# Kernel tuning notes

Hardware: AMD Instinct MI355X
Metric: run time of the kernel (lower is better)

The kernel has to match this reference:

```python
import jax, jax.numpy as jnp
import numpy as np
import math

B, L, H, NH = 4, 1024, 512, 8
D = H // NH

def setup_inputs() -> dict:
    key = jax.random.key(0)
    ks = jax.random.split(key, 12)
    s = 1.0 / math.sqrt(H)
    return {
        "key": jax.random.normal(ks[0], (B, L, H), jnp.float32),
        "query": jax.random.normal(ks[1], (B, L, H), jnp.float32),
        "value": jax.random.normal(ks[2], (B, L, H), jnp.float32),
        "rel_pos_embedding": jax.random.normal(ks[3], (B, NH, L, L), jnp.float32),
        "wk_w": jax.random.normal(ks[4], (H, H), jnp.float32) * s,
        "wk_b": jnp.zeros((H,), jnp.float32),
        "wq_w": jax.random.normal(ks[5], (H, H), jnp.float32) * s,
        "wq_b": jnp.zeros((H,), jnp.float32),
        "wv_w": jax.random.normal(ks[6], (H, H), jnp.float32) * s,
        "wv_b": jnp.zeros((H,), jnp.float32),
        "ff_w": jax.random.normal(ks[7], (H, H), jnp.float32) * s,
        "ff_b": jnp.zeros((H,), jnp.float32),
        "seq_len": jax.random.randint(ks[8], (B,), 1, 768, jnp.int32),
        "lex_num": jax.random.randint(ks[9], (B,), 0, 256, jnp.int32),
    }

def reference(key, query, value, rel_pos_embedding, wk_w, wk_b, wq_w, wq_b, wv_w, wv_b, ff_w, ff_b, seq_len, lex_num):
    b, l, h = key.shape
    # projections (torch Linear: x @ W^T + b)
    k = (key @ wk_w.T + wk_b).reshape(b, l, NH, D)
    q = (query @ wq_w.T + wq_b).reshape(b, l, NH, D)
    v = (value @ wv_w.T + wv_b).reshape(b, l, NH, D)
    # QK^T: [b, nh, lq, lk]
    scores = jnp.einsum("bqhd,bkhd->bhqk", q, k) / math.sqrt(D)
    scores = scores + rel_pos_embedding
    # padding mask over key positions
    lengths = (seq_len + lex_num).astype(jnp.int32)  # [b]
    mask = jnp.arange(l, dtype=jnp.int32)[None, :] < lengths[:, None]  # [b, l]
    scores = jnp.where(mask[:, None, None, :], scores, jnp.float32(-1e15))
    attn = jax.nn.softmax(scores, axis=-1)
    out = jnp.einsum("bhqk,bkhd->bqhd", attn, v).reshape(b, l, h)
    out = out @ ff_w.T + ff_b
    return out
```

## Files before the change

### kernel.cpp

```cpp
#include <hip/hip_runtime.h>
#include <hip/hip_bf16.h>

typedef __attribute__((ext_vector_type(8))) short bf16x8;
typedef __attribute__((ext_vector_type(4))) float f32x4;

__device__ __forceinline__ unsigned short f2bf(float f) {
    return __builtin_bit_cast(unsigned short, __float2bfloat16(f));
}

typedef const __attribute__((address_space(1))) void gvoid;
typedef __attribute__((address_space(3))) void lvoid;
#define GLDS(g, s) __builtin_amdgcn_global_load_lds((gvoid*)(g), (lvoid*)(s), 16, 0, 0)

__device__ __forceinline__ void block_barrier() {
    asm volatile("" ::: "memory");
    __builtin_amdgcn_s_barrier();
    asm volatile("" ::: "memory");
}

__global__ __launch_bounds__(256) void proj_kernel(
    const float* __restrict__ query, const float* __restrict__ key_, const float* __restrict__ value,
    const float* __restrict__ wq_w, const float* __restrict__ wq_b,
    const float* __restrict__ wk_w, const float* __restrict__ wk_b,
    const float* __restrict__ wv_w, const float* __restrict__ wv_b,
    unsigned short* __restrict__ Qb, unsigned short* __restrict__ Kb, unsigned short* __restrict__ Vt)
{
    const int wid = (blockIdx.x & 7) * 96 + (blockIdx.x >> 3);
    const int z  = wid >> 8;
    const int rr = wid & 255;
    const int by = rr >> 3, bx = rr & 7;

    const float* X    = (z == 0) ? query : (z == 1) ? key_ : value;
    const float* W    = (z == 0) ? wq_w  : (z == 1) ? wk_w : wv_w;
    const float* bias = (z == 0) ? wq_b  : (z == 1) ? wk_b : wv_b;

    const int t = threadIdx.x;
    const int l = t & 63;
    const int w = t >> 6;
    const int wm = w >> 1, wn = w & 1;
    const int m0 = by * 128, n0 = bx * 64;

    __shared__ __align__(16) unsigned short As[128 * 32];
    __shared__ __align__(16) unsigned short Bs[64 * 32];

    f32x4 acc[4][2];
#pragma unroll
    for (int i = 0; i < 4; i++)
#pragma unroll
        for (int j = 0; j < 2; j++) acc[i][j] = (f32x4){0.f, 0.f, 0.f, 0.f};

    float4 ra[4], rb[2];
    auto LOAD = [&](int k0) {
#pragma unroll
        for (int i = 0; i < 4; i++) {
            int idx = t + 256 * i;
            int row = idx >> 3, c = idx & 7;
            ra[i] = *(const float4*)(X + (size_t)(m0 + row) * 512 + k0 + c * 4);
        }
#pragma unroll
        for (int i = 0; i < 2; i++) {
            int idx = t + 256 * i;
            int row = idx >> 3, c = idx & 7;
            rb[i] = *(const float4*)(W + (size_t)(n0 + row) * 512 + k0 + c * 4);
        }
    };
    LOAD(0);

    for (int k0 = 0; k0 < 512; k0 += 32) {
        if (k0) block_barrier();
#pragma unroll
        for (int i = 0; i < 4; i++) {
            int idx = t + 256 * i;
            int row = idx >> 3, c = idx & 7;
            __align__(8) unsigned short va[4] = {f2bf(ra[i].x), f2bf(ra[i].y), f2bf(ra[i].z), f2bf(ra[i].w)};
            *(uint2*)(As + row * 32 + (((c >> 1) ^ (row & 3)) * 8) + (c & 1) * 4) = *(uint2*)va;
        }
#pragma unroll
        for (int i = 0; i < 2; i++) {
            int idx = t + 256 * i;
            int row = idx >> 3, c = idx & 7;
            __align__(8) unsigned short vb[4] = {f2bf(rb[i].x), f2bf(rb[i].y), f2bf(rb[i].z), f2bf(rb[i].w)};
            *(uint2*)(Bs + row * 32 + (((c >> 1) ^ (row & 3)) * 8) + (c & 1) * 4) = *(uint2*)vb;
        }
        asm volatile("s_waitcnt lgkmcnt(0)" ::: "memory");
        block_barrier();
        if (k0 + 32 < 512) LOAD(k0 + 32);

        bf16x8 af[4], bfv[2];
#pragma unroll
        for (int mf = 0; mf < 4; mf++) {
            int row = wm * 64 + mf * 16 + (l & 15);
            af[mf] = *(const bf16x8*)(As + row * 32 + (((l >> 4) ^ (row & 3)) * 8));
        }
#pragma unroll
        for (int nf = 0; nf < 2; nf++) {
            int row = wn * 32 + nf * 16 + (l & 15);
            bfv[nf] = *(const bf16x8*)(Bs + row * 32 + (((l >> 4) ^ (row & 3)) * 8));
        }
#pragma unroll
        for (int mf = 0; mf < 4; mf++)
#pragma unroll
            for (int nf = 0; nf < 2; nf++)
                acc[mf][nf] = __builtin_amdgcn_mfma_f32_16x16x32_bf16(af[mf], bfv[nf], acc[mf][nf], 0, 0, 0);
    }

    if (z < 2) {
        unsigned short* dst = (z == 0) ? Qb : Kb;
#pragma unroll
        for (int nf = 0; nf < 2; nf++) {
            int n = n0 + wn * 32 + nf * 16 + (l & 15);
            float bv = bias[n];
            int h = n >> 6, d = n & 63;
#pragma unroll
            for (int mf = 0; mf < 4; mf++) {
                int mbase = m0 + wm * 64 + mf * 16 + 4 * (l >> 4);
                int bb = mbase >> 10;
#pragma unroll
                for (int r = 0; r < 4; r++) {
                    int lq = (mbase + r) & 1023;
                    dst[((size_t)(bb * 8 + h) * 1024 + lq) * 64 + d] = f2bf(acc[mf][nf][r] + bv);
                }
            }
        }
    } else {
#pragma unroll
        for (int nf = 0; nf < 2; nf++) {
            int n = n0 + wn * 32 + nf * 16 + (l & 15);
            float bv = bias[n];
            int h = n >> 6, d = n & 63;
#pragma unroll
            for (int mf = 0; mf < 4; mf++) {
                int mbase = m0 + wm * 64 + mf * 16 + 4 * (l >> 4);
                int bb = mbase >> 10;
                int lq0 = mbase & 1023;
                ushort4 pk;
                pk.x = f2bf(acc[mf][nf][0] + bv);
                pk.y = f2bf(acc[mf][nf][1] + bv);
                pk.z = f2bf(acc[mf][nf][2] + bv);
                pk.w = f2bf(acc[mf][nf][3] + bv);
                *(ushort4*)(Vt + ((size_t)(bb * 8 + h) * 64 + d) * 1024 + lq0) = pk;
            }
        }
    }
}

__global__ __launch_bounds__(256, 2) void attn_kernel(
    const unsigned short* __restrict__ Qb, const unsigned short* __restrict__ Kb,
    const unsigned short* __restrict__ Vt, const float* __restrict__ rel_pos,
    const int* __restrict__ seq_len, const int* __restrict__ lex_num,
    unsigned short* __restrict__ AO)
{
    const int t = threadIdx.x;
    const int l = t & 63;
    const int w = t >> 6;
    const int wid = (blockIdx.x & 7) * 64 + (blockIdx.x >> 3);
    const int x8 = wid >> 6;
    const int g  = (wid >> 4) & 3;
    const int qt = wid & 15;
    const int b  = g;
    const int h  = (x8 + 2 * g) & 7;
    const int q0 = qt * 64;
    const int bh = b * 8 + h;
    const int len = seq_len[b] + lex_num[b];
    const int nkt = (len + 127) >> 7;

    __shared__ __align__(16) unsigned short Qs[64 * 64];
    __shared__ __align__(16) unsigned short Ks[2][128 * 64];
    __shared__ __align__(16) unsigned short Vs[64 * 128];
    __shared__ __align__(16) unsigned short Ps[4 * 16 * 128];

    const unsigned short* Qg = Qb + ((size_t)bh * 1024 + q0) * 64;
    const unsigned short* Kg = Kb + (size_t)bh * 1024 * 64;
    const unsigned short* Vg = Vt + (size_t)bh * 64 * 1024;
    const float* Rg = rel_pos + ((size_t)bh * 1024 + q0) * 1024;

    const int rl8 = l >> 3, c8 = l & 7;
    const int kvc = (c8 ^ rl8) * 8;
    const int rl4 = l >> 4, c16 = l & 15;

    auto STAGE_K = [&](int kt2, int nb) {
        const int k0s = kt2 * 128;
#pragma unroll
        for (int j = 0; j < 4; j++) {
            int row = j * 32 + w * 8 + rl8;
            GLDS(Kg + (size_t)(k0s + row) * 64 + kvc, &Ks[nb][(j * 32 + w * 8) * 64]);
        }
    };
    auto STAGE_V = [&](int kt2) {
        const int k0s = kt2 * 128;
#pragma unroll
        for (int j = 0; j < 4; j++) {
            int drow = j * 16 + w * 4 + rl4;
            int sc = (c16 ^ (w * 4 + rl4)) * 8;
            GLDS(Vg + (size_t)drow * 1024 + k0s + sc, &Vs[(j * 16 + w * 4) * 128]);
        }
    };
    auto RELLOAD = [&](float (&R)[32], int kt2) {
        const float* rp = Rg + (size_t)(w * 16 + 4 * (l >> 4)) * 1024 + kt2 * 128 + (l & 15);
#pragma unroll
        for (int r = 0; r < 4; r++)
#pragma unroll
            for (int kn = 0; kn < 8; kn++)
                R[r * 8 + kn] = rp[(size_t)r * 1024 + kn * 16];
    };

    float rA[32], rB[32];
#pragma unroll
    for (int j = 0; j < 2; j++) {
        int row = w * 16 + j * 8 + rl8;
        GLDS(Qg + (size_t)row * 64 + kvc, &Qs[(w * 16 + j * 8) * 64]);
    }
    STAGE_K(0, 0);
    RELLOAD(rA, 0);
    STAGE_V(0);

    bf16x8 qf[2];
    f32x4 oacc[4];
#pragma unroll
    for (int dn = 0; dn < 4; dn++) oacc[dn] = (f32x4){0.f, 0.f, 0.f, 0.f};
    float l_run[4] = {0.f, 0.f, 0.f, 0.f};
    unsigned short* Pw = Ps + w * 16 * 128;

    auto tile_body = [&](int kt, float (&REL)[32], float (&RELN)[32]) {
        const int cur = kt & 1;
        const int k0 = kt * 128;
        if (kt + 1 < nkt) {
            STAGE_K(kt + 1, cur ^ 1);
            RELLOAD(RELN, kt + 1);
            asm volatile("s_waitcnt vmcnt(40)" ::: "memory");
        } else {
            asm volatile("s_waitcnt vmcnt(4)" ::: "memory");
        }
        block_barrier();

        if (kt == 0) {
#pragma unroll
            for (int s = 0; s < 2; s++) {
                int row = w * 16 + (l & 15);
                int ch = 4 * s + (l >> 4);
                qf[s] = *(const bf16x8*)(Qs + row * 64 + ((ch ^ (row & 7)) * 8));
            }
        }

        const unsigned short* Ksc = Ks[cur];

        f32x4 sa[8];
#pragma unroll
        for (int kn = 0; kn < 8; kn++) sa[kn] = (f32x4){0.f, 0.f, 0.f, 0.f};
        __builtin_amdgcn_s_setprio(1);
#pragma unroll
        for (int s = 0; s < 2; s++)
#pragma unroll
            for (int kn = 0; kn < 8; kn++) {
                int krow = kn * 16 + (l & 15);
                int ch = 4 * s + (l >> 4);
                bf16x8 kf = *(const bf16x8*)(Ksc + krow * 64 + ((ch ^ (krow & 7)) * 8));
                sa[kn] = __builtin_amdgcn_mfma_f32_16x16x32_bf16(qf[s], kf, sa[kn], 0, 0, 0);
            }
        __builtin_amdgcn_s_setprio(0);

#pragma unroll
        for (int r = 0; r < 4; r++) {
            int qrow = 4 * (l >> 4) + r;
            float pr[8], rs = 0.f;
#pragma unroll
            for (int kn = 0; kn < 8; kn++) {
                int kg = k0 + kn * 16 + (l & 15);
                float x = sa[kn][r] * 0.125f + REL[r * 8 + kn] - 16.0f;
                pr[kn] = (kg < len) ? __expf(x) : 0.0f;
                rs += pr[kn];
            }
#pragma unroll
            for (int o = 1; o < 16; o <<= 1) rs += __shfl_xor(rs, o, 64);
            l_run[r] += rs;
#pragma unroll
            for (int kn = 0; kn < 8; kn++) {
                int ck = (kn * 2 + ((l >> 3) & 1)) ^ (qrow & 15);
                Pw[qrow * 128 + ck * 8 + (l & 7)] = f2bf(pr[kn]);
            }
        }

        if (kt + 1 < nkt) {
            asm volatile("s_waitcnt vmcnt(36)" ::: "memory");
        } else {
            asm volatile("s_waitcnt vmcnt(0)" ::: "memory");
        }
        block_barrier();

        __builtin_amdgcn_s_setprio(1);
#pragma unroll
        for (int s = 0; s < 4; s++) {
            int arow = (l & 15);
            bf16x8 pf = *(const bf16x8*)(Pw + arow * 128 + (((s * 4 + (l >> 4)) ^ arow) * 8));
#pragma unroll
            for (int dn = 0; dn < 4; dn++) {
                int drow = dn * 16 + (l & 15);
                bf16x8 vf = *(const bf16x8*)(Vs + drow * 128 + (((s * 4 + (l >> 4)) ^ (drow & 15)) * 8));
                oacc[dn] = __builtin_amdgcn_mfma_f32_16x16x32_bf16(pf, vf, oacc[dn], 0, 0, 0);
            }
        }
        __builtin_amdgcn_s_setprio(0);
        block_barrier();
        if (kt + 1 < nkt) STAGE_V(kt + 1);
    };

    for (int kt = 0; kt < nkt; kt += 2) {
        tile_body(kt, rA, rB);
        if (kt + 1 < nkt) tile_body(kt + 1, rB, rA);
    }

    unsigned short* AOg = AO + ((size_t)(b * 1024 + q0 + w * 16)) * 512 + h * 64;
#pragma unroll
    for (int r = 0; r < 4; r++) {
        float inv = 1.0f / l_run[r];
        int qrow = 4 * (l >> 4) + r;
#pragma unroll
        for (int dn = 0; dn < 4; dn++)
            AOg[(size_t)qrow * 512 + dn * 16 + (l & 15)] = f2bf(oacc[dn][r] * inv);
    }
}

__global__ __launch_bounds__(256) void ff_kernel(
    const unsigned short* __restrict__ AO, const float* __restrict__ ff_w,
    const float* __restrict__ ff_b, float* __restrict__ out)
{
    const int t = threadIdx.x;
    const int l = t & 63;
    const int w = t >> 6;
    const int wm = w >> 1, wn = w & 1;
    const int wid = (blockIdx.x & 7) * 64 + (blockIdx.x >> 3);
    const int by = wid >> 3;
    const int bx = wid & 7;
    const int m0 = by * 64, n0 = bx * 64;

    __shared__ __align__(16) unsigned short As[64 * 32];
    __shared__ __align__(16) unsigned short Bs[64 * 32];

    f32x4 acc[2][2];
#pragma unroll
    for (int i = 0; i < 2; i++)
#pragma unroll
        for (int j = 0; j < 2; j++) acc[i][j] = (f32x4){0.f, 0.f, 0.f, 0.f};

    uint4 ua;
    float4 rbf[2];
    const int arow = t >> 2, ac = t & 3;
    auto LOAD = [&](int k0) {
        ua = *(const uint4*)(AO + (size_t)(m0 + arow) * 512 + k0 + ac * 8);
#pragma unroll
        for (int i = 0; i < 2; i++) {
            int idx = t + 256 * i;
            int row = idx >> 3, c = idx & 7;
            rbf[i] = *(const float4*)(ff_w + (size_t)(n0 + row) * 512 + k0 + c * 4);
        }
    };
    LOAD(0);

    for (int k0 = 0; k0 < 512; k0 += 32) {
        if (k0) block_barrier();
        *(uint4*)(As + arow * 32 + ((ac ^ (arow & 3)) * 8)) = ua;
#pragma unroll
        for (int i = 0; i < 2; i++) {
            int idx = t + 256 * i;
            int row = idx >> 3, c = idx & 7;
            __align__(8) unsigned short vb[4] = {f2bf(rbf[i].x), f2bf(rbf[i].y), f2bf(rbf[i].z), f2bf(rbf[i].w)};
            *(uint2*)(Bs + row * 32 + (((c >> 1) ^ (row & 3)) * 8) + (c & 1) * 4) = *(uint2*)vb;
        }
        asm volatile("s_waitcnt lgkmcnt(0)" ::: "memory");
        block_barrier();
        if (k0 + 32 < 512) LOAD(k0 + 32);

        bf16x8 af[2], bfv[2];
#pragma unroll
        for (int mf = 0; mf < 2; mf++) {
            int row = wm * 32 + mf * 16 + (l & 15);
            af[mf] = *(const bf16x8*)(As + row * 32 + (((l >> 4) ^ (row & 3)) * 8));
        }
#pragma unroll
        for (int nf = 0; nf < 2; nf++) {
            int row = wn * 32 + nf * 16 + (l & 15);
            bfv[nf] = *(const bf16x8*)(Bs + row * 32 + (((l >> 4) ^ (row & 3)) * 8));
        }
#pragma unroll
        for (int mf = 0; mf < 2; mf++)
#pragma unroll
            for (int nf = 0; nf < 2; nf++)
                acc[mf][nf] = __builtin_amdgcn_mfma_f32_16x16x32_bf16(af[mf], bfv[nf], acc[mf][nf], 0, 0, 0);
    }

#pragma unroll
    for (int nf = 0; nf < 2; nf++) {
        int n = n0 + wn * 32 + nf * 16 + (l & 15);
        float bv = ff_b[n];
#pragma unroll
        for (int mf = 0; mf < 2; mf++) {
            int mbase = m0 + wm * 32 + mf * 16 + 4 * (l >> 4);
#pragma unroll
            for (int r = 0; r < 4; r++)
                out[(size_t)(mbase + r) * 512 + n] = acc[mf][nf][r] + bv;
        }
    }
}

extern "C" void kernel_launch(void* const* d_in, const int* in_sizes, int n_in,
                              void* d_out, int out_size, void* d_ws, size_t ws_size,
                              hipStream_t stream) {
    const float* key   = (const float*)d_in[0];
    const float* query = (const float*)d_in[1];
    const float* value = (const float*)d_in[2];
    const float* rel   = (const float*)d_in[3];
    const float* wk_w  = (const float*)d_in[4];
    const float* wk_b  = (const float*)d_in[5];
    const float* wq_w  = (const float*)d_in[6];
    const float* wq_b  = (const float*)d_in[7];
    const float* wv_w  = (const float*)d_in[8];
    const float* wv_b  = (const float*)d_in[9];
    const float* ff_w  = (const float*)d_in[10];
    const float* ff_b  = (const float*)d_in[11];
    const int* seq_len = (const int*)d_in[12];
    const int* lex_num = (const int*)d_in[13];
    float* out = (float*)d_out;

    unsigned short* Qb = (unsigned short*)d_ws;
    unsigned short* Kb = Qb + 2097152;
    unsigned short* Vt = Kb + 2097152;
    unsigned short* AO = Vt + 2097152;

    proj_kernel<<<dim3(768), 256, 0, stream>>>(query, key, value,
                                               wq_w, wq_b, wk_w, wk_b, wv_w, wv_b,
                                               Qb, Kb, Vt);
    attn_kernel<<<dim3(512), 256, 0, stream>>>(Qb, Kb, Vt, rel, seq_len, lex_num, AO);
    ff_kernel<<<dim3(512), 256, 0, stream>>>(AO, ff_w, ff_b, out);
}
```

Before: 57.52 us.

## Stage fp32 projection tiles via async global-to-LDS loads with double buffering

The projection GEMM now loads fp32 tiles of X and W straight into LDS with global_load_lds into two ping-pong buffers, using an XOR swizzle. The bf16 conversion moves to after the LDS read, where each thread converts its own fragments. The goal is to overlap the next tile's global load with the current MFMA work and to drop the register round-trip and conversion stores. In exchange it uses twice the LDS (fp32, double-buffered), which can lower occupancy, repeats the conversions per wave, and adds a second barrier per iteration.

```diff
diff --git a/kernel.cpp b/kernel.cpp
--- a/kernel.cpp
+++ b/kernel.cpp
@@ -40,8 +40,8 @@
     const int wm = w >> 1, wn = w & 1;
     const int m0 = by * 128, n0 = bx * 64;
 
-    __shared__ __align__(16) unsigned short As[128 * 32];
-    __shared__ __align__(16) unsigned short Bs[64 * 32];
+    __shared__ __align__(16) float Asf[2][128 * 32];
+    __shared__ __align__(16) float Bsf[2][64 * 32];
 
     f32x4 acc[4][2];
 #pragma unroll
@@ -49,59 +49,66 @@
 #pragma unroll
         for (int j = 0; j < 2; j++) acc[i][j] = (f32x4){0.f, 0.f, 0.f, 0.f};
 
-    float4 ra[4], rb[2];
-    auto LOAD = [&](int k0) {
-#pragma unroll
-        for (int i = 0; i < 4; i++) {
-            int idx = t + 256 * i;
-            int row = idx >> 3, c = idx & 7;
-            ra[i] = *(const float4*)(X + (size_t)(m0 + row) * 512 + k0 + c * 4);
-        }
-#pragma unroll
-        for (int i = 0; i < 2; i++) {
-            int idx = t + 256 * i;
-            int row = idx >> 3, c = idx & 7;
-            rb[i] = *(const float4*)(W + (size_t)(n0 + row) * 512 + k0 + c * 4);
-        }
-    };
-    LOAD(0);
-
-    for (int k0 = 0; k0 < 512; k0 += 32) {
-        if (k0) block_barrier();
-#pragma unroll
-        for (int i = 0; i < 4; i++) {
-            int idx = t + 256 * i;
-            int row = idx >> 3, c = idx & 7;
-            __align__(8) unsigned short va[4] = {f2bf(ra[i].x), f2bf(ra[i].y), f2bf(ra[i].z), f2bf(ra[i].w)};
-            *(uint2*)(As + row * 32 + (((c >> 1) ^ (row & 3)) * 8) + (c & 1) * 4) = *(uint2*)va;
-        }
-#pragma unroll
-        for (int i = 0; i < 2; i++) {
-            int idx = t + 256 * i;
-            int row = idx >> 3, c = idx & 7;
-            __align__(8) unsigned short vb[4] = {f2bf(rb[i].x), f2bf(rb[i].y), f2bf(rb[i].z), f2bf(rb[i].w)};
-            *(uint2*)(Bs + row * 32 + (((c >> 1) ^ (row & 3)) * 8) + (c & 1) * 4) = *(uint2*)vb;
-        }
-        asm volatile("s_waitcnt lgkmcnt(0)" ::: "memory");
-        block_barrier();
-        if (k0 + 32 < 512) LOAD(k0 + 32);
+    const int rl8 = l >> 3, c8 = l & 7;
+    const int csrc = (c8 ^ rl8) * 4;
+
+    auto STAGE = [&](int kt, int nb) {
+        const int k0 = kt * 32;
+#pragma unroll
+        for (int j = 0; j < 4; j++) {
+            int row = j * 32 + w * 8 + rl8;
+            GLDS(X + (size_t)(m0 + row) * 512 + k0 + csrc, &Asf[nb][(j * 32 + w * 8) * 32]);
+        }
+#pragma unroll
+        for (int j = 0; j < 2; j++) {
+            int row = j * 32 + w * 8 + rl8;
+            GLDS(W + (size_t)(n0 + row) * 512 + k0 + csrc, &Bsf[nb][(j * 32 + w * 8) * 32]);
+        }
+    };
+
+    STAGE(0, 0);
+
+    for (int kt = 0; kt < 16; kt++) {
+        const int cur = kt & 1;
+        if (kt + 1 < 16) {
+            STAGE(kt + 1, cur ^ 1);
+            asm volatile("s_waitcnt vmcnt(6)" ::: "memory");
+        } else {
+            asm volatile("s_waitcnt vmcnt(0)" ::: "memory");
+        }
+        block_barrier();
+
+        const float* Ac = Asf[cur];
+        const float* Bc = Bsf[cur];
+        const int ch2 = 2 * (l >> 4);
+        const int s = l & 7;
 
         bf16x8 af[4], bfv[2];
 #pragma unroll
         for (int mf = 0; mf < 4; mf++) {
             int row = wm * 64 + mf * 16 + (l & 15);
-            af[mf] = *(const bf16x8*)(As + row * 32 + (((l >> 4) ^ (row & 3)) * 8));
+            float4 lo = *(const float4*)(Ac + row * 32 + ((ch2 ^ s) * 4));
+            float4 hi = *(const float4*)(Ac + row * 32 + (((ch2 + 1) ^ s) * 4));
+            __align__(16) unsigned short v[8] = {f2bf(lo.x), f2bf(lo.y), f2bf(lo.z), f2bf(lo.w),
+                                                 f2bf(hi.x), f2bf(hi.y), f2bf(hi.z), f2bf(hi.w)};
+            af[mf] = *(const bf16x8*)v;
         }
 #pragma unroll
         for (int nf = 0; nf < 2; nf++) {
             int row = wn * 32 + nf * 16 + (l & 15);
-            bfv[nf] = *(const bf16x8*)(Bs + row * 32 + (((l >> 4) ^ (row & 3)) * 8));
+            float4 lo = *(const float4*)(Bc + row * 32 + ((ch2 ^ s) * 4));
+            float4 hi = *(const float4*)(Bc + row * 32 + (((ch2 + 1) ^ s) * 4));
+            __align__(16) unsigned short v[8] = {f2bf(lo.x), f2bf(lo.y), f2bf(lo.z), f2bf(lo.w),
+                                                 f2bf(hi.x), f2bf(hi.y), f2bf(hi.z), f2bf(hi.w)};
+            bfv[nf] = *(const bf16x8*)v;
         }
 #pragma unroll
         for (int mf = 0; mf < 4; mf++)
 #pragma unroll
             for (int nf = 0; nf < 2; nf++)
                 acc[mf][nf] = __builtin_amdgcn_mfma_f32_16x16x32_bf16(af[mf], bfv[nf], acc[mf][nf], 0, 0, 0);
+
+        block_barrier();
     }
 
     if (z < 2) {
```

After: 60.35 us. +4.9%, slower.
